# Optimization experiments

Measured on AMD Instinct MI355X. Metric: run time of the kernel, lower is better.

The kernel has to match this reference:

```python
import jax, jax.numpy as jnp
import numpy as np
import math

B, C, L = 16, 2048, 64

def setup_inputs() -> dict:
    key = jax.random.key(0)
    kq, kk, kv = jax.random.split(key, 3)
    q = jax.random.normal(kq, (B, C, L), dtype=jnp.float32)
    k = jax.random.normal(kk, (B, C, L), dtype=jnp.float32)
    v = jax.random.normal(kv, (B, C, L), dtype=jnp.float32)
    return {"q": q, "k": k, "v": v}

def reference(q, k, v):
    b, c, l = q.shape
    # Faithful to the torch source: k is RESHAPED (row-major), not transposed.
    k_t = k.reshape(b, l, c)                      # (b, l, c)
    score = jnp.matmul(q, k_t) / math.sqrt(l)     # (b, c, c)
    # nn.Softmax() with no dim on a 3D tensor -> torch implicit dim = 0 (batch axis)
    score = jax.nn.softmax(score, axis=0)
    return jnp.matmul(score, v)                   # (b, c, l)
```

## Files before the change

### kernel.cpp

```cpp
#include <hip/hip_runtime.h>

typedef __attribute__((ext_vector_type(8))) short short8;
typedef __attribute__((ext_vector_type(4))) float float4v;

#define BATCH 16
#define CDIM 2048
#define LDIM 64
#define BSTRIDE (CDIM * LDIM)

__device__ __forceinline__ float bf2f(unsigned short u) {
    return __uint_as_float(((unsigned int)u) << 16);
}
__device__ __forceinline__ unsigned short f2bf(float f) {
    unsigned int x = __float_as_uint(f);
    x += 0x7fffu + ((x >> 16) & 1u);
    return (unsigned short)(x >> 16);
}
__device__ __forceinline__ void dma16(const void* g, void* l) {
    __builtin_amdgcn_global_load_lds(
        (const __attribute__((address_space(1))) void*)g,
        (__attribute__((address_space(3))) void*)l, 16, 0, 0);
}

__global__ __launch_bounds__(256) void prepass_kernel(
    const float* __restrict__ q, const float* __restrict__ k, const float* __restrict__ v,
    float* __restrict__ out, unsigned short* __restrict__ qb,
    unsigned short* __restrict__ kT, unsigned short* __restrict__ vS)
{
    __shared__ float tile[32][33];
    const int bx = blockIdx.x;
    const int tid = threadIdx.x;
    if (bx < 2048) {
        ((float4v*)out)[bx * 256 + tid] = (float4v){0.f, 0.f, 0.f, 0.f};
    } else if (bx < 3072) {
        int i = (bx - 2048) * 256 + tid;
        const float4v* src = (const float4v*)q + (size_t)i * 2;
        float4v x0 = src[0], x1 = src[1];
        unsigned int u0 = f2bf(x0[0] * 0.125f) | ((unsigned)f2bf(x0[1] * 0.125f) << 16);
        unsigned int u1 = f2bf(x0[2] * 0.125f) | ((unsigned)f2bf(x0[3] * 0.125f) << 16);
        unsigned int u2 = f2bf(x1[0] * 0.125f) | ((unsigned)f2bf(x1[1] * 0.125f) << 16);
        unsigned int u3 = f2bf(x1[2] * 0.125f) | ((unsigned)f2bf(x1[3] * 0.125f) << 16);
        int b = i >> 14, r = i & 16383, m = r >> 3, j = r & 7;
        *(uint4*)(qb + (size_t)b * BSTRIDE + m * 64 + (j ^ (m & 7)) * 8) =
            make_uint4(u0, u1, u2, u3);
    } else if (bx < 5120) {
        int idx = bx - 3072; int b = idx >> 7, t = idx & 127;
        int c0 = (t >> 1) * 32, r0 = (t & 1) * 32;
        const float* src = k + (size_t)b * BSTRIDE;
        unsigned short* dst = kT + (size_t)b * BSTRIDE;
        int tx = tid & 31, ty = tid >> 5;
#pragma unroll
        for (int p = 0; p < 4; p++)
            tile[ty + p * 8][tx] = src[(size_t)(r0 + ty + p * 8) * 2048 + c0 + tx];
        __syncthreads();
#pragma unroll
        for (int p = 0; p < 4; p++) {
            int n = c0 + ty + p * 8, ic = r0 + tx, j = ic >> 3;
            dst[(size_t)n * 64 + (j ^ (n & 7)) * 8 + (tx & 7)] = f2bf(tile[tx][ty + p * 8]);
        }
    } else {
        int idx = bx - 5120; int b = idx >> 7, t = idx & 127;
        int c0 = (t & 1) * 32, r0 = (t >> 1) * 32;
        const float* src = v + (size_t)b * BSTRIDE;
        unsigned short* dst = vS + (size_t)b * BSTRIDE;
        int tx = tid & 31, ty = tid >> 5;
#pragma unroll
        for (int p = 0; p < 4; p++)
            tile[ty + p * 8][tx] = src[(size_t)(r0 + ty + p * 8) * 64 + c0 + tx];
        __syncthreads();
#pragma unroll
        for (int p = 0; p < 4; p++) {
            int j = c0 + ty + p * 8, nb = r0 >> 5, qc = tx >> 3;
            dst[(size_t)nb * 2048 + j * 32 + (qc ^ (j & 3)) * 8 + (tx & 7)] =
                f2bf(tile[tx][ty + p * 8]);
        }
    }
}

__global__ __launch_bounds__(256, 2) void dinv_kernel(
    const unsigned short* __restrict__ qb, const unsigned short* __restrict__ kT,
    unsigned short* __restrict__ Dt)
{
    __shared__ unsigned short Sq[8192];
    __shared__ unsigned short Sk[4096];
    const int tid = threadIdx.x, w = tid >> 6, lane = tid & 63;
    const int c = lane & 15, q = lane >> 4;
    const int mt = blockIdx.x & 15, ng = blockIdx.x >> 4;
    const int m0 = mt * 128, n0 = ng * 64;

    float4v Dacc[2][4];
#pragma unroll
    for (int ms = 0; ms < 2; ms++)
#pragma unroll
        for (int nt = 0; nt < 4; nt++) Dacc[ms][nt] = (float4v){0.f, 0.f, 0.f, 0.f};

    for (int b = 0; b < BATCH; b++) {
        __syncthreads();
        const char* qg = (const char*)(qb + (size_t)b * BSTRIDE + (size_t)m0 * 64);
        const char* kg = (const char*)(kT + (size_t)b * BSTRIDE + (size_t)n0 * 64);
#pragma unroll
        for (int kk = 0; kk < 4; kk++)
            dma16(qg + (w * 4 + kk) * 1024 + lane * 16, (char*)Sq + (w * 4 + kk) * 1024);
        dma16(kg + (w * 2 + 0) * 1024 + lane * 16, (char*)Sk + (w * 2 + 0) * 1024);
        dma16(kg + (w * 2 + 1) * 1024 + lane * 16, (char*)Sk + (w * 2 + 1) * 1024);
        asm volatile("s_waitcnt vmcnt(0)" ::: "memory");
        __syncthreads();

        short8 Qf[2][2];
#pragma unroll
        for (int ms = 0; ms < 2; ms++)
#pragma unroll
            for (int h = 0; h < 2; h++)
                Qf[ms][h] = *(const short8*)&Sq[(w * 32 + ms * 16 + c) * 64 +
                                                ((h * 4 + q) ^ (c & 7)) * 8];
#pragma unroll
        for (int nt = 0; nt < 4; nt++) {
            short8 A0 = *(const short8*)&Sk[(nt * 16 + c) * 64 + (q ^ (c & 7)) * 8];
            short8 A1 = *(const short8*)&Sk[(nt * 16 + c) * 64 + ((4 + q) ^ (c & 7)) * 8];
#pragma unroll
            for (int ms = 0; ms < 2; ms++) {
                float4v d = (float4v){0.f, 0.f, 0.f, 0.f};
                d = __builtin_amdgcn_mfma_f32_16x16x32_bf16(A0, Qf[ms][0], d, 0, 0, 0);
                d = __builtin_amdgcn_mfma_f32_16x16x32_bf16(A1, Qf[ms][1], d, 0, 0, 0);
#pragma unroll
                for (int r = 0; r < 4; r++) Dacc[ms][nt][r] += __expf(d[r]);
            }
        }
    }
#pragma unroll
    for (int ms = 0; ms < 2; ms++)
#pragma unroll
        for (int nt = 0; nt < 4; nt++) {
            int m_local = w * 32 + ms * 16 + c;
            int T = mt * 64 + ng * 2 + (nt >> 1);
            int j = (nt & 1) * 4 + q;
            ushort4 o;
#pragma unroll
            for (int r = 0; r < 4; r++) o[r] = f2bf(1.f / Dacc[ms][nt][r]);
            *(ushort4*)&Dt[(size_t)T * 4096 + m_local * 32 + (j ^ (c & 7)) * 4] = o;
        }
}

__global__ __launch_bounds__(256, 4) void attn_main_kernel(
    const unsigned short* __restrict__ qb, const unsigned short* __restrict__ kT,
    const unsigned short* __restrict__ vS, const unsigned short* __restrict__ Dt,
    float* __restrict__ out)
{
    __shared__ unsigned short Sk[2048];
    __shared__ unsigned short Sv[2048];
    __shared__ unsigned short Sd[4096];
    __shared__ unsigned short Ep[4][2][16][40];

    const int tid = threadIdx.x, w = tid >> 6, lane = tid & 63;
    const int c = lane & 15, q = lane >> 4;
    const int b = blockIdx.x & 15, mt = (blockIdx.x >> 4) & 15, ns = blockIdx.x >> 8;
    const int m0 = mt * 128, nbase = ns * 512;

    const unsigned short* qb_b = qb + (size_t)b * BSTRIDE;
    const char* kbase = (const char*)(kT + (size_t)b * BSTRIDE);
    const char* vbase = (const char*)(vS + (size_t)b * BSTRIDE);

    short8 Qf[2][2];
#pragma unroll
    for (int ms = 0; ms < 2; ms++)
#pragma unroll
        for (int h = 0; h < 2; h++)
            Qf[ms][h] = *(const short8*)(qb_b + (m0 + w * 32 + ms * 16 + c) * 64 +
                                         ((h * 4 + q) ^ (c & 7)) * 8);
    float4v acc[2][4];
#pragma unroll
    for (int ms = 0; ms < 2; ms++)
#pragma unroll
        for (int jt = 0; jt < 4; jt++) acc[ms][jt] = (float4v){0.f, 0.f, 0.f, 0.f};

    for (int st = 0; st < 16; st++) {
        const int n0 = nbase + st * 32;
        const int T = mt * 64 + ns * 16 + st;
        __syncthreads();
        dma16(kbase + (size_t)n0 * 128 + w * 1024 + lane * 16, (char*)Sk + w * 1024);
        dma16(vbase + (size_t)(ns * 16 + st) * 4096 + w * 1024 + lane * 16,
              (char*)Sv + w * 1024);
        dma16((const char*)Dt + (size_t)T * 8192 + w * 1024 + lane * 16,
              (char*)Sd + w * 1024);
        dma16((const char*)Dt + (size_t)T * 8192 + (w + 4) * 1024 + lane * 16,
              (char*)Sd + (w + 4) * 1024);
        asm volatile("s_waitcnt vmcnt(0)" ::: "memory");
        __syncthreads();

#pragma unroll
        for (int nt = 0; nt < 2; nt++) {
            short8 A0 = *(const short8*)&Sk[(nt * 16 + c) * 64 + (q ^ (c & 7)) * 8];
            short8 A1 = *(const short8*)&Sk[(nt * 16 + c) * 64 + ((4 + q) ^ (c & 7)) * 8];
#pragma unroll
            for (int ms = 0; ms < 2; ms++) {
                float4v d = (float4v){0.f, 0.f, 0.f, 0.f};
                d = __builtin_amdgcn_mfma_f32_16x16x32_bf16(A0, Qf[ms][0], d, 0, 0, 0);
                d = __builtin_amdgcn_mfma_f32_16x16x32_bf16(A1, Qf[ms][1], d, 0, 0, 0);
                uint2 du = *(const uint2*)&Sd[(w * 32 + ms * 16 + c) * 32 +
                                              (((nt * 4 + q) ^ (c & 7)) * 4)];
                float d0 = __uint_as_float(du.x << 16);
                float d1 = __uint_as_float(du.x & 0xffff0000u);
                float d2 = __uint_as_float(du.y << 16);
                float d3 = __uint_as_float(du.y & 0xffff0000u);
                ushort4 e;
                e.x = f2bf(__expf(d[0]) * d0);
                e.y = f2bf(__expf(d[1]) * d1);
                e.z = f2bf(__expf(d[2]) * d2);
                e.w = f2bf(__expf(d[3]) * d3);
                *(ushort4*)&Ep[w][ms][c][nt * 16 + q * 4] = e;
            }
        }
        asm volatile("s_waitcnt lgkmcnt(0)" ::: "memory");

#pragma unroll
        for (int ms = 0; ms < 2; ms++) {
            short8 Pf = *(const short8*)&Ep[w][ms][c][q * 8];
#pragma unroll
            for (int jt = 0; jt < 4; jt++) {
                short8 Vf = *(const short8*)&Sv[(jt * 16 + c) * 32 + (q ^ (c & 3)) * 8];
                acc[ms][jt] = __builtin_amdgcn_mfma_f32_16x16x32_bf16(Pf, Vf, acc[ms][jt], 0, 0, 0);
            }
        }
    }

#pragma unroll
    for (int ms = 0; ms < 2; ms++)
#pragma unroll
        for (int jt = 0; jt < 4; jt++)
#pragma unroll
            for (int r = 0; r < 4; r++) {
                int m = m0 + w * 32 + ms * 16 + q * 4 + r;
                atomicAdd(&out[((size_t)b * CDIM + m) * LDIM + jt * 16 + c], acc[ms][jt][r]);
            }
}

extern "C" void kernel_launch(void* const* d_in, const int* in_sizes, int n_in,
                              void* d_out, int out_size, void* d_ws, size_t ws_size,
                              hipStream_t stream) {
    const float* q = (const float*)d_in[0];
    const float* k = (const float*)d_in[1];
    const float* v = (const float*)d_in[2];
    float* out = (float*)d_out;

    unsigned short* qb = (unsigned short*)d_ws;
    unsigned short* kT = qb + (size_t)BATCH * BSTRIDE;
    unsigned short* vS = kT + (size_t)BATCH * BSTRIDE;
    unsigned short* Dt = vS + (size_t)BATCH * BSTRIDE;

    prepass_kernel<<<7168, 256, 0, stream>>>(q, k, v, out, qb, kT, vS);
    dinv_kernel<<<512, 256, 0, stream>>>(qb, kT, Dt);
    attn_main_kernel<<<1024, 256, 0, stream>>>(qb, kT, vS, Dt, out);
}
```

Before: 139.6 us.

## Double-buffer LDS loads in dinv and attention kernels, restructure prepass transposes

Both the dinv and main attention kernels now double-buffer their K/Q/V shared-memory tiles, prefetching the next batch or step via global_load_lds while computing on the current one, with partial vmcnt waits and raw s_barriers. The reciprocal-denominator buffer is rewritten in a per-lane register-friendly layout so the main kernel loads it directly into registers instead of staging it through LDS. The prepass uses fewer, larger blocks with 64x64 bf16 tiles and vectorized 16-byte stores for the K and V transposes. This raises LDS usage, which may lower occupancy, and relies on hand-tuned wait counts for correctness.

```diff
diff --git a/kernel.cpp b/kernel.cpp
--- a/kernel.cpp
+++ b/kernel.cpp
@@ -27,13 +27,16 @@
     float* __restrict__ out, unsigned short* __restrict__ qb,
     unsigned short* __restrict__ kT, unsigned short* __restrict__ vS)
 {
-    __shared__ float tile[32][33];
+    __shared__ unsigned short T[64][68];
     const int bx = blockIdx.x;
-    const int tid = threadIdx.x;
-    if (bx < 2048) {
-        ((float4v*)out)[bx * 256 + tid] = (float4v){0.f, 0.f, 0.f, 0.f};
-    } else if (bx < 3072) {
-        int i = (bx - 2048) * 256 + tid;
+    const int t = threadIdx.x;
+
+    if (bx < 1024) {
+        float4v z = (float4v){0.f, 0.f, 0.f, 0.f};
+        float4v* o = (float4v*)out + (size_t)bx * 512 + t * 2;
+        o[0] = z; o[1] = z;
+    } else if (bx < 2048) {
+        int i = (bx - 1024) * 256 + t;
         const float4v* src = (const float4v*)q + (size_t)i * 2;
         float4v x0 = src[0], x1 = src[1];
         unsigned int u0 = f2bf(x0[0] * 0.125f) | ((unsigned)f2bf(x0[1] * 0.125f) << 16);
@@ -43,36 +46,54 @@
         int b = i >> 14, r = i & 16383, m = r >> 3, j = r & 7;
         *(uint4*)(qb + (size_t)b * BSTRIDE + m * 64 + (j ^ (m & 7)) * 8) =
             make_uint4(u0, u1, u2, u3);
-    } else if (bx < 5120) {
-        int idx = bx - 3072; int b = idx >> 7, t = idx & 127;
-        int c0 = (t >> 1) * 32, r0 = (t & 1) * 32;
-        const float* src = k + (size_t)b * BSTRIDE;
+    } else if (bx < 2560) {
+        int idx = bx - 2048, b = idx >> 5, n0 = (idx & 31) * 64;
+        const float* src = k + (size_t)b * BSTRIDE + (size_t)(t >> 2) * 2048 + n0 + (t & 3) * 16;
+#pragma unroll
+        for (int kk = 0; kk < 4; kk++) {
+            float4v x = *(const float4v*)(src + kk * 4);
+#pragma unroll
+            for (int e = 0; e < 4; e++)
+                T[t >> 2][(t & 3) * 16 + kk * 4 + e] = f2bf(x[e]);
+        }
+        __syncthreads();
         unsigned short* dst = kT + (size_t)b * BSTRIDE;
-        int tx = tid & 31, ty = tid >> 5;
-#pragma unroll
-        for (int p = 0; p < 4; p++)
-            tile[ty + p * 8][tx] = src[(size_t)(r0 + ty + p * 8) * 2048 + c0 + tx];
+        int n = t & 63;
+#pragma unroll
+        for (int jj = 0; jj < 2; jj++) {
+            int j = (t >> 6) * 2 + jj;
+            ushort4 g0, g1;
+#pragma unroll
+            for (int e = 0; e < 4; e++) { g0[e] = T[j * 8 + e][n]; g1[e] = T[j * 8 + 4 + e][n]; }
+            *(uint4*)(dst + (size_t)(n0 + n) * 64 + (j ^ (n & 7)) * 8) =
+                make_uint4(g0.x | ((unsigned)g0.y << 16), g0.z | ((unsigned)g0.w << 16),
+                           g1.x | ((unsigned)g1.y << 16), g1.z | ((unsigned)g1.w << 16));
+        }
+    } else {
+        int idx = bx - 2560, b = idx >> 5, n0 = (idx & 31) * 64;
+        const float* src = v + (size_t)b * BSTRIDE + (size_t)(t >> 2) * 64 + n0 * 0 + (t & 3) * 16;
+        src += (size_t)n0 * 64;
+#pragma unroll
+        for (int kk = 0; kk < 4; kk++) {
+            float4v x = *(const float4v*)(src + kk * 4);
+#pragma unroll
+            for (int e = 0; e < 4; e++)
+                T[t >> 2][(t & 3) * 16 + kk * 4 + e] = f2bf(x[e]);
+        }
         __syncthreads();
-#pragma unroll
-        for (int p = 0; p < 4; p++) {
-            int n = c0 + ty + p * 8, ic = r0 + tx, j = ic >> 3;
-            dst[(size_t)n * 64 + (j ^ (n & 7)) * 8 + (tx & 7)] = f2bf(tile[tx][ty + p * 8]);
-        }
-    } else {
-        int idx = bx - 5120; int b = idx >> 7, t = idx & 127;
-        int c0 = (t & 1) * 32, r0 = (t >> 1) * 32;
-        const float* src = v + (size_t)b * BSTRIDE;
         unsigned short* dst = vS + (size_t)b * BSTRIDE;
-        int tx = tid & 31, ty = tid >> 5;
-#pragma unroll
-        for (int p = 0; p < 4; p++)
-            tile[ty + p * 8][tx] = src[(size_t)(r0 + ty + p * 8) * 64 + c0 + tx];
-        __syncthreads();
-#pragma unroll
-        for (int p = 0; p < 4; p++) {
-            int j = c0 + ty + p * 8, nb = r0 >> 5, qc = tx >> 3;
-            dst[(size_t)nb * 2048 + j * 32 + (qc ^ (j & 3)) * 8 + (tx & 7)] =
-                f2bf(tile[tx][ty + p * 8]);
+        int j = t & 63, qc = t >> 6;
+#pragma unroll
+        for (int nb = 0; nb < 2; nb++) {
+            ushort4 g0, g1;
+#pragma unroll
+            for (int e = 0; e < 4; e++) {
+                g0[e] = T[nb * 32 + qc * 8 + e][j];
+                g1[e] = T[nb * 32 + qc * 8 + 4 + e][j];
+            }
+            *(uint4*)(dst + (size_t)(n0 / 32 + nb) * 2048 + j * 32 + (qc ^ (j & 3)) * 8) =
+                make_uint4(g0.x | ((unsigned)g0.y << 16), g0.z | ((unsigned)g0.w << 16),
+                           g1.x | ((unsigned)g1.y << 16), g1.z | ((unsigned)g1.w << 16));
         }
     }
 }
@@ -81,8 +102,8 @@
     const unsigned short* __restrict__ qb, const unsigned short* __restrict__ kT,
     unsigned short* __restrict__ Dt)
 {
-    __shared__ unsigned short Sq[8192];
-    __shared__ unsigned short Sk[4096];
+    __shared__ unsigned short Sq[2][8192];
+    __shared__ unsigned short Sk[2][4096];
     const int tid = threadIdx.x, w = tid >> 6, lane = tid & 63;
     const int c = lane & 15, q = lane >> 4;
     const int mt = blockIdx.x & 15, ng = blockIdx.x >> 4;
@@ -94,29 +115,43 @@
 #pragma unroll
         for (int nt = 0; nt < 4; nt++) Dacc[ms][nt] = (float4v){0.f, 0.f, 0.f, 0.f};
 
-    for (int b = 0; b < BATCH; b++) {
-        __syncthreads();
-        const char* qg = (const char*)(qb + (size_t)b * BSTRIDE + (size_t)m0 * 64);
-        const char* kg = (const char*)(kT + (size_t)b * BSTRIDE + (size_t)n0 * 64);
+    {
+        const char* qg = (const char*)(qb + (size_t)m0 * 64);
+        const char* kg = (const char*)(kT + (size_t)n0 * 64);
 #pragma unroll
         for (int kk = 0; kk < 4; kk++)
-            dma16(qg + (w * 4 + kk) * 1024 + lane * 16, (char*)Sq + (w * 4 + kk) * 1024);
-        dma16(kg + (w * 2 + 0) * 1024 + lane * 16, (char*)Sk + (w * 2 + 0) * 1024);
-        dma16(kg + (w * 2 + 1) * 1024 + lane * 16, (char*)Sk + (w * 2 + 1) * 1024);
-        asm volatile("s_waitcnt vmcnt(0)" ::: "memory");
-        __syncthreads();
+            dma16(qg + (w * 4 + kk) * 1024 + lane * 16, (char*)Sq[0] + (w * 4 + kk) * 1024);
+        dma16(kg + (w * 2 + 0) * 1024 + lane * 16, (char*)Sk[0] + (w * 2 + 0) * 1024);
+        dma16(kg + (w * 2 + 1) * 1024 + lane * 16, (char*)Sk[0] + (w * 2 + 1) * 1024);
+    }
+
+    for (int bb = 0; bb < BATCH; bb++) {
+        const int p = bb & 1;
+        if (bb < BATCH - 1) {
+            const char* qg = (const char*)(qb + (size_t)(bb + 1) * BSTRIDE + (size_t)m0 * 64);
+            const char* kg = (const char*)(kT + (size_t)(bb + 1) * BSTRIDE + (size_t)n0 * 64);
+#pragma unroll
+            for (int kk = 0; kk < 4; kk++)
+                dma16(qg + (w * 4 + kk) * 1024 + lane * 16, (char*)Sq[p ^ 1] + (w * 4 + kk) * 1024);
+            dma16(kg + (w * 2 + 0) * 1024 + lane * 16, (char*)Sk[p ^ 1] + (w * 2 + 0) * 1024);
+            dma16(kg + (w * 2 + 1) * 1024 + lane * 16, (char*)Sk[p ^ 1] + (w * 2 + 1) * 1024);
+            asm volatile("s_waitcnt vmcnt(6)" ::: "memory");
+        } else {
+            asm volatile("s_waitcnt vmcnt(0)" ::: "memory");
+        }
+        asm volatile("s_barrier" ::: "memory");
 
         short8 Qf[2][2];
 #pragma unroll
         for (int ms = 0; ms < 2; ms++)
 #pragma unroll
             for (int h = 0; h < 2; h++)
-                Qf[ms][h] = *(const short8*)&Sq[(w * 32 + ms * 16 + c) * 64 +
-                                                ((h * 4 + q) ^ (c & 7)) * 8];
+                Qf[ms][h] = *(const short8*)&Sq[p][(w * 32 + ms * 16 + c) * 64 +
+                                                  ((h * 4 + q) ^ (c & 7)) * 8];
 #pragma unroll
         for (int nt = 0; nt < 4; nt++) {
-            short8 A0 = *(const short8*)&Sk[(nt * 16 + c) * 64 + (q ^ (c & 7)) * 8];
-            short8 A1 = *(const short8*)&Sk[(nt * 16 + c) * 64 + ((4 + q) ^ (c & 7)) * 8];
+            short8 A0 = *(const short8*)&Sk[p][(nt * 16 + c) * 64 + (q ^ (c & 7)) * 8];
+            short8 A1 = *(const short8*)&Sk[p][(nt * 16 + c) * 64 + ((4 + q) ^ (c & 7)) * 8];
 #pragma unroll
             for (int ms = 0; ms < 2; ms++) {
                 float4v d = (float4v){0.f, 0.f, 0.f, 0.f};
@@ -126,18 +161,20 @@
                 for (int r = 0; r < 4; r++) Dacc[ms][nt][r] += __expf(d[r]);
             }
         }
-    }
+        asm volatile("s_barrier" ::: "memory");
+    }
+
 #pragma unroll
     for (int ms = 0; ms < 2; ms++)
 #pragma unroll
         for (int nt = 0; nt < 4; nt++) {
-            int m_local = w * 32 + ms * 16 + c;
-            int T = mt * 64 + ng * 2 + (nt >> 1);
-            int j = (nt & 1) * 4 + q;
-            ushort4 o;
-#pragma unroll
-            for (int r = 0; r < 4; r++) o[r] = f2bf(1.f / Dacc[ms][nt][r]);
-            *(ushort4*)&Dt[(size_t)T * 4096 + m_local * 32 + (j ^ (c & 7)) * 4] = o;
+            unsigned int x = f2bf(1.f / Dacc[ms][nt][0]) |
+                             ((unsigned)f2bf(1.f / Dacc[ms][nt][1]) << 16);
+            unsigned int y = f2bf(1.f / Dacc[ms][nt][2]) |
+                             ((unsigned)f2bf(1.f / Dacc[ms][nt][3]) << 16);
+            size_t T = (size_t)(mt * 64 + ng * 2 + (nt >> 1));
+            *(uint2*)((char*)Dt + T * 8192 + w * 2048 + (ms * 2 + (nt & 1)) * 512 + lane * 8) =
+                make_uint2(x, y);
         }
 }
 
@@ -146,9 +183,8 @@
     const unsigned short* __restrict__ vS, const unsigned short* __restrict__ Dt,
     float* __restrict__ out)
 {
-    __shared__ unsigned short Sk[2048];
-    __shared__ unsigned short Sv[2048];
-    __shared__ unsigned short Sd[4096];
+    __shared__ unsigned short Sk[2][2048];
+    __shared__ unsigned short Sv[2][2048];
     __shared__ unsigned short Ep[4][2][16][40];
 
     const int tid = threadIdx.x, w = tid >> 6, lane = tid & 63;
@@ -173,54 +209,62 @@
 #pragma unroll
         for (int jt = 0; jt < 4; jt++) acc[ms][jt] = (float4v){0.f, 0.f, 0.f, 0.f};
 
+    dma16(kbase + (size_t)nbase * 128 + w * 1024 + lane * 16, (char*)Sk[0] + w * 1024);
+    dma16(vbase + (size_t)(ns * 16) * 4096 + w * 1024 + lane * 16, (char*)Sv[0] + w * 1024);
+
     for (int st = 0; st < 16; st++) {
-        const int n0 = nbase + st * 32;
-        const int T = mt * 64 + ns * 16 + st;
-        __syncthreads();
-        dma16(kbase + (size_t)n0 * 128 + w * 1024 + lane * 16, (char*)Sk + w * 1024);
-        dma16(vbase + (size_t)(ns * 16 + st) * 4096 + w * 1024 + lane * 16,
-              (char*)Sv + w * 1024);
-        dma16((const char*)Dt + (size_t)T * 8192 + w * 1024 + lane * 16,
-              (char*)Sd + w * 1024);
-        dma16((const char*)Dt + (size_t)T * 8192 + (w + 4) * 1024 + lane * 16,
-              (char*)Sd + (w + 4) * 1024);
-        asm volatile("s_waitcnt vmcnt(0)" ::: "memory");
-        __syncthreads();
+        const int p = st & 1;
+        if (st < 15) {
+            const int n1 = nbase + (st + 1) * 32;
+            dma16(kbase + (size_t)n1 * 128 + w * 1024 + lane * 16, (char*)Sk[p ^ 1] + w * 1024);
+            dma16(vbase + (size_t)(ns * 16 + st + 1) * 4096 + w * 1024 + lane * 16,
+                  (char*)Sv[p ^ 1] + w * 1024);
+            asm volatile("s_waitcnt vmcnt(2)" ::: "memory");
+        } else {
+            asm volatile("s_waitcnt vmcnt(0)" ::: "memory");
+        }
+        asm volatile("s_barrier" ::: "memory");
+
+        const char* dtb = (const char*)Dt + (size_t)(mt * 64 + ns * 16 + st) * 8192 +
+                          w * 2048 + lane * 8;
+        uint2 du[2][2];
+        du[0][0] = *(const uint2*)(dtb + 0);
+        du[0][1] = *(const uint2*)(dtb + 512);
+        du[1][0] = *(const uint2*)(dtb + 1024);
+        du[1][1] = *(const uint2*)(dtb + 1536);
 
 #pragma unroll
         for (int nt = 0; nt < 2; nt++) {
-            short8 A0 = *(const short8*)&Sk[(nt * 16 + c) * 64 + (q ^ (c & 7)) * 8];
-            short8 A1 = *(const short8*)&Sk[(nt * 16 + c) * 64 + ((4 + q) ^ (c & 7)) * 8];
+            short8 A0 = *(const short8*)&Sk[p][(nt * 16 + c) * 64 + (q ^ (c & 7)) * 8];
+            short8 A1 = *(const short8*)&Sk[p][(nt * 16 + c) * 64 + ((4 + q) ^ (c & 7)) * 8];
 #pragma unroll
             for (int ms = 0; ms < 2; ms++) {
                 float4v d = (float4v){0.f, 0.f, 0.f, 0.f};
                 d = __builtin_amdgcn_mfma_f32_16x16x32_bf16(A0, Qf[ms][0], d, 0, 0, 0);
                 d = __builtin_amdgcn_mfma_f32_16x16x32_bf16(A1, Qf[ms][1], d, 0, 0, 0);
-                uint2 du = *(const uint2*)&Sd[(w * 32 + ms * 16 + c) * 32 +
-                                              (((nt * 4 + q) ^ (c & 7)) * 4)];
-                float d0 = __uint_as_float(du.x << 16);
-                float d1 = __uint_as_float(du.x & 0xffff0000u);
-                float d2 = __uint_as_float(du.y << 16);
-                float d3 = __uint_as_float(du.y & 0xffff0000u);
+                uint2 u2 = du[ms][nt];
                 ushort4 e;
-                e.x = f2bf(__expf(d[0]) * d0);
-                e.y = f2bf(__expf(d[1]) * d1);
-                e.z = f2bf(__expf(d[2]) * d2);
-                e.w = f2bf(__expf(d[3]) * d3);
+                e.x = f2bf(__expf(d[0]) * __uint_as_float(u2.x << 16));
+                e.y = f2bf(__expf(d[1]) * __uint_as_float(u2.x & 0xffff0000u));
+                e.z = f2bf(__expf(d[2]) * __uint_as_float(u2.y << 16));
+                e.w = f2bf(__expf(d[3]) * __uint_as_float(u2.y & 0xffff0000u));
                 *(ushort4*)&Ep[w][ms][c][nt * 16 + q * 4] = e;
             }
         }
         asm volatile("s_waitcnt lgkmcnt(0)" ::: "memory");
 
+        short8 Vf[4];
+#pragma unroll
+        for (int jt = 0; jt < 4; jt++)
+            Vf[jt] = *(const short8*)&Sv[p][(jt * 16 + c) * 32 + (q ^ (c & 3)) * 8];
 #pragma unroll
         for (int ms = 0; ms < 2; ms++) {
             short8 Pf = *(const short8*)&Ep[w][ms][c][q * 8];
 #pragma unroll
-            for (int jt = 0; jt < 4; jt++) {
-                short8 Vf = *(const short8*)&Sv[(jt * 16 + c) * 32 + (q ^ (c & 3)) * 8];
-                acc[ms][jt] = __builtin_amdgcn_mfma_f32_16x16x32_bf16(Pf, Vf, acc[ms][jt], 0, 0, 0);
-            }
-        }
+            for (int jt = 0; jt < 4; jt++)
+                acc[ms][jt] = __builtin_amdgcn_mfma_f32_16x16x32_bf16(Pf, Vf[jt], acc[ms][jt], 0, 0, 0);
+        }
+        asm volatile("s_barrier" ::: "memory");
     }
 
 #pragma unroll
@@ -247,7 +291,7 @@
     unsigned short* vS = kT + (size_t)BATCH * BSTRIDE;
     unsigned short* Dt = vS + (size_t)BATCH * BSTRIDE;
 
-    prepass_kernel<<<7168, 256, 0, stream>>>(q, k, v, out, qb, kT, vS);
+    prepass_kernel<<<3072, 256, 0, stream>>>(q, k, v, out, qb, kT, vS);
     dinv_kernel<<<512, 256, 0, stream>>>(qb, kT, Dt);
     attn_main_kernel<<<1024, 256, 0, stream>>>(qb, kT, vS, Dt, out);
 }
```

Measured after the change: 140.7 us. Within noise of the previous version (+0.7%).
